# Optimization experiments

Measured on AMD Instinct MI355X. Metric: run time of the kernel, lower is better.

## Reference

```python
import jax, jax.numpy as jnp
import numpy as np

B, N, F, FE, H, C = 2, 2048, 128, 8, 4, 64
LEAKY_ALPHA = 0.2
NEG_INF = -1e9


def setup_inputs() -> dict:
    key = jax.random.key(0)
    ks = jax.random.split(key, 8)
    return {
        "X": jax.random.normal(ks[0], (B, N, F), jnp.float32),
        "A": jax.random.uniform(ks[1], (B, N, N), jnp.float32),
        "E": jax.random.normal(ks[2], (B, N, N, FE), jnp.float32),
        "W_edge": jax.random.normal(ks[3], (FE, 1), jnp.float32) * 0.1,
        "b_edge": jnp.zeros((1,), jnp.float32),
        "W_gat": jax.random.normal(ks[4], (H, F, C), jnp.float32) * 0.05,
        "a_src": jax.random.normal(ks[5], (H, C), jnp.float32) * 0.1,
        "a_dst": jax.random.normal(ks[6], (H, C), jnp.float32) * 0.1,
        "b_gat": jnp.zeros((H * C,), jnp.float32),
        "ln_gamma": jnp.ones((H * C,), jnp.float32),
        "ln_beta": jnp.zeros((H * C,), jnp.float32),
    }


def reference(X, A, E, W_edge, b_edge, W_gat, a_src, a_dst, b_gat, ln_gamma, ln_beta):
    # --- edge gate: sigmoid(Dense_1(E)) -> [B,N,N], multiply into adjacency ---
    edge_w = jax.nn.sigmoid(jnp.einsum("bije,eo->bijo", E, W_edge) + b_edge)
    A = A * edge_w[..., 0]  # [B,N,N]

    # --- multi-head dense GAT (spektral GATConv, concat_heads, elu) ---
    h = jnp.einsum("bnf,hfc->bnhc", X, W_gat)  # [B,N,H,C]
    s_src = jnp.einsum("bnhc,hc->bnh", h, a_src)  # [B,N,H]
    s_dst = jnp.einsum("bnhc,hc->bnh", h, a_dst)
    # e_ij = LeakyReLU(src_i + dst_j): [B,N(i),N(j),H]
    logits = jax.nn.leaky_relu(s_src[:, :, None, :] + s_dst[:, None, :, :],
                               negative_slope=LEAKY_ALPHA)
    mask = jnp.where(A == 0.0, NEG_INF, 0.0)[..., None]  # [B,N,N,1]
    attn = jax.nn.softmax(logits + mask, axis=2)  # softmax over neighbors j
    out = jnp.einsum("bijh,bjhc->bihc", attn, h)  # [B,N,H,C]
    out = out.reshape(B, N, H * C) + b_gat
    out = jax.nn.elu(out)

    # --- LayerNorm over the feature axis (inference: dropout is identity) ---
    mu = jnp.mean(out, axis=-1, keepdims=True)
    var = jnp.var(out, axis=-1, keepdims=True)
    out = (out - mu) * jax.lax.rsqrt(var + 1e-3) * ln_gamma + ln_beta
    return out
```

## Files before the change

### kernel.cpp

```cpp
#include <hip/hip_runtime.h>
#include <hip/hip_bf16.h>


#define BB 2
#define NN 2048
#define FF 128
#define HH 4
#define CC 64
#define HC 256
#define TN 8
#define JB (NN / 8)
#define LOG2E 1.4426950408889634f

typedef __attribute__((ext_vector_type(8))) short short8;
typedef __attribute__((ext_vector_type(4))) float f32x4;

__device__ __forceinline__ float wave_sum(float v) {
#pragma unroll
    for (int m = 32; m >= 1; m >>= 1) v += __shfl_xor(v, m, 64);
    return v;
}

__device__ __forceinline__ unsigned short bf16rne(float x) {
    unsigned u = __float_as_uint(x);
    return (unsigned short)((u + 0x7fffu + ((u >> 16) & 1u)) >> 16);
}

__global__ __launch_bounds__(256) void k1_proj(
    const float* __restrict__ X, const float* __restrict__ Adj,
    const float* __restrict__ Wg,
    const float* __restrict__ a_src, const float* __restrict__ a_dst,
    unsigned short* __restrict__ hT, float* __restrict__ ssT,
    float* __restrict__ sdT, unsigned char* __restrict__ zT)
{
    const int blk = blockIdx.x;
    const int b  = blk / (NN / TN);
    const int n0 = (blk % (NN / TN)) * TN;
    const int tid = threadIdx.x;
    const int h = tid >> 6, c = tid & 63;

    float hv[TN];
#pragma unroll
    for (int r = 0; r < TN; ++r) hv[r] = 0.f;

    const float* xp = X + (size_t)(b * NN + n0) * FF;

#pragma unroll 4
    for (int f4 = 0; f4 < FF / 4; ++f4) {
        const int f = f4 * 4;
        const float w0 = Wg[(h * FF + f + 0) * CC + c];
        const float w1 = Wg[(h * FF + f + 1) * CC + c];
        const float w2 = Wg[(h * FF + f + 2) * CC + c];
        const float w3 = Wg[(h * FF + f + 3) * CC + c];
#pragma unroll
        for (int r = 0; r < TN; ++r) {
            float4 x4 = *(const float4*)(xp + r * FF + f);
            hv[r] = fmaf(x4.x, w0, hv[r]);
            hv[r] = fmaf(x4.y, w1, hv[r]);
            hv[r] = fmaf(x4.z, w2, hv[r]);
            hv[r] = fmaf(x4.w, w3, hv[r]);
        }
    }

    union { short8 v; unsigned short u[8]; } pk;
#pragma unroll
    for (int r = 0; r < TN; ++r) pk.u[r] = bf16rne(hv[r]);
    *(short8*)&hT[((((size_t)b * HH + h) * JB + (n0 >> 3)) * CC + c) * 8] = pk.v;

    const float as = a_src[tid];
    const float ad = a_dst[tid];
#pragma unroll
    for (int r = 0; r < TN; ++r) {
        const int n = n0 + r;
        float s1 = wave_sum(hv[r] * as);
        float s2 = wave_sum(hv[r] * ad);
        if (c == 0) {
            ssT[(b * HH + h) * NN + n] = s1 * LOG2E;
            sdT[(b * HH + h) * NN + n] = s2 * LOG2E;
        }
    }

    {
        const int r = tid >> 5;
        const int s = tid & 31;
        const size_t row = (size_t)(b * NN + n0 + r);
        const float* ap = Adj + row * NN + s * 64;
        unsigned char* zp = zT + (row << 8);
#pragma unroll
        for (int k = 0; k < 8; ++k) {
            float4 a0 = *(const float4*)(ap + k * 8);
            float4 a1 = *(const float4*)(ap + k * 8 + 4);
            unsigned m = 0u;
            m |= (a0.x == 0.f) ? 1u   : 0u;
            m |= (a0.y == 0.f) ? 2u   : 0u;
            m |= (a0.z == 0.f) ? 4u   : 0u;
            m |= (a0.w == 0.f) ? 8u   : 0u;
            m |= (a1.x == 0.f) ? 16u  : 0u;
            m |= (a1.y == 0.f) ? 32u  : 0u;
            m |= (a1.z == 0.f) ? 64u  : 0u;
            m |= (a1.w == 0.f) ? 128u : 0u;
            const int jb = s * 8 + k;
            const int jq = jb >> 6, rem = jb & 63;
            const int it = rem >> 2, lq = rem & 3;
            zp[jq * 64 + lq * 16 + it] = (unsigned char)m;
        }
    }
}

struct Stage {
    float4 sda, sdb;
    short8 bfr[4];
};

__device__ __forceinline__ void load_stage(
    Stage& s, const float* sdp, const unsigned short* hb, int it)
{
    const int js = it * 32;
    s.sda = *(const float4*)(sdp + js);
    s.sdb = *(const float4*)(sdp + js + 4);
    const unsigned short* hp = hb + it * 2048;
#pragma unroll
    for (int ni = 0; ni < 4; ++ni)
        s.bfr[ni] = *(const short8*)(hp + ni * 128);
}

__device__ __forceinline__ void consume_stage(
    const Stage& s, float ss, bool wz,
    unsigned long long mlo, unsigned long long mhi, int it,
    f32x4* acc, f32x4& accS, short8 onesv)
{
    const float sd[8] = {s.sda.x, s.sda.y, s.sda.z, s.sda.w,
                         s.sdb.x, s.sdb.y, s.sdb.z, s.sdb.w};
    float p[8];
    __builtin_amdgcn_s_setprio(1);
#pragma unroll
    for (int t = 0; t < 8; ++t) {
        float x = ss + sd[t];
        x = fmaxf(x, 0.2f * x);
        p[t] = __builtin_amdgcn_exp2f(x);
    }
    if (wz) {
        const unsigned mb =
            (unsigned)(((it & 8) ? mhi : mlo) >> ((it & 7) * 8)) & 0xffu;
        if (__any(mb != 0u)) {
#pragma unroll
            for (int t = 0; t < 8; ++t)
                if ((mb >> t) & 1u) p[t] = 0.f;
        }
    }
    union { short8 v; __hip_bfloat162 h2[4]; } pk;
#pragma unroll
    for (int t = 0; t < 4; ++t)
        pk.h2[t] = __float22bfloat162_rn(make_float2(p[2 * t], p[2 * t + 1]));
    accS = __builtin_amdgcn_mfma_f32_16x16x32_bf16(pk.v, onesv, accS, 0, 0, 0);
#pragma unroll
    for (int ni = 0; ni < 4; ++ni)
        acc[ni] = __builtin_amdgcn_mfma_f32_16x16x32_bf16(pk.v, s.bfr[ni], acc[ni], 0, 0, 0);
    __builtin_amdgcn_s_setprio(0);
}

__global__ __launch_bounds__(1024, 4) void k2_attn(
    const unsigned short* __restrict__ hT, const float* __restrict__ ssT,
    const float* __restrict__ sdT, const unsigned char* __restrict__ zT,
    const float* __restrict__ b_gat, const float* __restrict__ gamma,
    const float* __restrict__ beta, float* __restrict__ out)
{
    __shared__ float accs[3][16][HH][64];
    __shared__ float lsumx[4][HH][16];

    const int blk = blockIdx.x;
    const int b  = blk >> 7;
    const int i0 = (blk & 127) << 4;
    const int tid  = threadIdx.x;
    const int wave = tid >> 6;
    const int h  = wave & 3;
    const int jq = wave >> 2;
    const int l  = tid & 63;
    const int lr = l & 15;
    const int lq = l >> 4;

    const float ss = ssT[(b * HH + h) * NN + i0 + lr];

    const uint4 mw = *(const uint4*)(zT + ((size_t)(b * NN + i0 + lr) << 8)
                                       + jq * 64 + lq * 16);
    const unsigned long long mlo = ((unsigned long long)mw.y << 32) | mw.x;
    const unsigned long long mhi = ((unsigned long long)mw.w << 32) | mw.z;
    const bool wz = __any((mlo | mhi) != 0ull);

    short8 onesv;
#pragma unroll
    for (int i = 0; i < 8; ++i) onesv[i] = (short)0x3F80;

    f32x4 acc[4];
#pragma unroll
    for (int ni = 0; ni < 4; ++ni) acc[ni] = (f32x4){0.f, 0.f, 0.f, 0.f};
    f32x4 accS = (f32x4){0.f, 0.f, 0.f, 0.f};

    const float* sdp = sdT + (b * HH + h) * NN + jq * 512 + lq * 8;
    const unsigned short* hb =
        hT + ((((size_t)b * HH + h) * JB + jq * 64 + lq) * CC + lr) * 8;

    Stage s0, s1;
    load_stage(s0, sdp, hb, 0);
    load_stage(s1, sdp, hb, 1);
#pragma unroll 1
    for (int it = 0; it < 16; it += 2) {
        consume_stage(s0, ss, wz, mlo, mhi, it, acc, accS, onesv);
        if (it + 2 < 16) load_stage(s0, sdp, hb, it + 2);
        consume_stage(s1, ss, wz, mlo, mhi, it + 1, acc, accS, onesv);
        if (it + 3 < 16) load_stage(s1, sdp, hb, it + 3);
    }

    if (lr == 0)
#pragma unroll
        for (int r = 0; r < 4; ++r) lsumx[jq][h][lq * 4 + r] = accS[r];

    if (jq > 0) {
#pragma unroll
        for (int ni = 0; ni < 4; ++ni)
#pragma unroll
            for (int r = 0; r < 4; ++r)
                accs[jq - 1][ni * 4 + r][h][l] = acc[ni][r];
    }
    __syncthreads();

    float vals[4][4];
    if (jq == 0) {
        const float lcomb = lsumx[0][h][lr] + lsumx[1][h][lr]
                          + lsumx[2][h][lr] + lsumx[3][h][lr];
        float lrow[4];
#pragma unroll
        for (int r = 0; r < 4; ++r) lrow[r] = __shfl(lcomb, lq * 4 + r, 64);

        float bg[4];
#pragma unroll
        for (int ni = 0; ni < 4; ++ni) bg[ni] = b_gat[h * 64 + ni * 16 + lr];

#pragma unroll
        for (int ni = 0; ni < 4; ++ni)
#pragma unroll
            for (int r = 0; r < 4; ++r) {
                float a = acc[ni][r] + accs[0][ni * 4 + r][h][l]
                        + accs[1][ni * 4 + r][h][l] + accs[2][ni * 4 + r][h][l];
                float v = a / lrow[r] + bg[ni];
                vals[ni][r] = (v > 0.f) ? v : (__expf(v) - 1.f);
            }
    }
    __syncthreads();

    float* vbuf = &accs[0][0][0][0];
    if (jq == 0) {
#pragma unroll
        for (int ni = 0; ni < 4; ++ni)
#pragma unroll
            for (int r = 0; r < 4; ++r)
                vbuf[((h * 4 + ni) * 16 + (lq * 4 + r)) * 16 + lr] = vals[ni][r];
    }
    __syncthreads();

    {
        const int row = wave;
        const int h2  = l >> 4;
        const int ni2 = (l >> 2) & 3;
        const int lr0 = (l & 3) * 4;
        float4 v4 = *(const float4*)&vbuf[((h2 * 4 + ni2) * 16 + row) * 16 + lr0];

        float S1 = wave_sum(v4.x + v4.y + v4.z + v4.w);
        float S2 = wave_sum(v4.x * v4.x + v4.y * v4.y + v4.z * v4.z + v4.w * v4.w);
        float mu  = S1 * (1.f / HC);
        float var = S2 * (1.f / HC) - mu * mu;
        float inv = rsqrtf(var + 1e-3f);

        float4 gm = *(const float4*)&gamma[l * 4];
        float4 bm = *(const float4*)&beta[l * 4];
        float4 o;
        o.x = (v4.x - mu) * inv * gm.x + bm.x;
        o.y = (v4.y - mu) * inv * gm.y + bm.y;
        o.z = (v4.z - mu) * inv * gm.z + bm.z;
        o.w = (v4.w - mu) * inv * gm.w + bm.w;
        *(float4*)(out + (size_t)(b * NN + i0 + row) * HC + l * 4) = o;
    }
}

extern "C" void kernel_launch(void* const* d_in, const int* in_sizes, int n_in,
                              void* d_out, int out_size, void* d_ws, size_t ws_size,
                              hipStream_t stream)
{
    const float* X     = (const float*)d_in[0];
    const float* Adj   = (const float*)d_in[1];
    const float* Wg    = (const float*)d_in[5];
    const float* a_src = (const float*)d_in[6];
    const float* a_dst = (const float*)d_in[7];
    const float* b_gat = (const float*)d_in[8];
    const float* gam   = (const float*)d_in[9];
    const float* bet   = (const float*)d_in[10];
    float* out = (float*)d_out;

    const size_t hT_elems = (size_t)BB * HH * CC * NN;
    const size_t ss_elems = (size_t)BB * HH * NN;

    unsigned short* hT = (unsigned short*)d_ws;
    float* ssT = (float*)(hT + hT_elems);
    float* sdT = ssT + ss_elems;
    unsigned char* zT = (unsigned char*)(sdT + ss_elems);

    k1_proj<<<BB * NN / TN, 256, 0, stream>>>(X, Adj, Wg, a_src, a_dst, hT, ssT, sdT, zT);
    k2_attn<<<BB * (NN / 16), 1024, 0, stream>>>(hT, ssT, sdT, zT, b_gat, gam, bet, out);
}
```

Measured before the change: 370.4 us.

## Split attention blocks by j-quarter across row tiles and reduce partials in new kernel

Each attention block used to cover 16 rows with four waves splitting the neighbor range, then combine the four partial sums in shared memory and apply the norm. Now each block covers 64 rows for a single neighbor quarter, so the four row subgroups share the same hT and sdT stream, which improves reuse of those loads. Partial numerators and denominators are written to global workspace, and a third kernel sums them, then applies bias, ELU and LayerNorm. This drops the in-block syncs and shared-memory reduction, at the cost of an extra launch and roughly 16 MB of partial-sum traffic to global memory.

```diff
diff --git a/kernel.cpp b/kernel.cpp
--- a/kernel.cpp
+++ b/kernel.cpp
@@ -162,27 +162,26 @@
 __global__ __launch_bounds__(1024, 4) void k2_attn(
     const unsigned short* __restrict__ hT, const float* __restrict__ ssT,
     const float* __restrict__ sdT, const unsigned char* __restrict__ zT,
-    const float* __restrict__ b_gat, const float* __restrict__ gamma,
-    const float* __restrict__ beta, float* __restrict__ out)
-{
-    __shared__ float accs[3][16][HH][64];
-    __shared__ float lsumx[4][HH][16];
-
+    float* __restrict__ Pacc, float* __restrict__ Pden)
+{
     const int blk = blockIdx.x;
-    const int b  = blk >> 7;
-    const int i0 = (blk & 127) << 4;
+    const int b     = blk >> 7;
+    const int itile = (blk >> 2) & 31;
+    const int jqB   = blk & 3;
+    const int i0    = itile * 64;
     const int tid  = threadIdx.x;
     const int wave = tid >> 6;
-    const int h  = wave & 3;
-    const int jq = wave >> 2;
+    const int h    = wave & 3;
+    const int isub = wave >> 2;
     const int l  = tid & 63;
     const int lr = l & 15;
     const int lq = l >> 4;
-
-    const float ss = ssT[(b * HH + h) * NN + i0 + lr];
-
-    const uint4 mw = *(const uint4*)(zT + ((size_t)(b * NN + i0 + lr) << 8)
-                                       + jq * 64 + lq * 16);
+    const int irow0 = i0 + isub * 16;
+
+    const float ss = ssT[(b * HH + h) * NN + irow0 + lr];
+
+    const uint4 mw = *(const uint4*)(zT + ((size_t)(b * NN + irow0 + lr) << 8)
+                                       + jqB * 64 + lq * 16);
     const unsigned long long mlo = ((unsigned long long)mw.y << 32) | mw.x;
     const unsigned long long mhi = ((unsigned long long)mw.w << 32) | mw.z;
     const bool wz = __any((mlo | mhi) != 0ull);
@@ -196,9 +195,9 @@
     for (int ni = 0; ni < 4; ++ni) acc[ni] = (f32x4){0.f, 0.f, 0.f, 0.f};
     f32x4 accS = (f32x4){0.f, 0.f, 0.f, 0.f};
 
-    const float* sdp = sdT + (b * HH + h) * NN + jq * 512 + lq * 8;
+    const float* sdp = sdT + (b * HH + h) * NN + jqB * 512 + lq * 8;
     const unsigned short* hb =
-        hT + ((((size_t)b * HH + h) * JB + jq * 64 + lq) * CC + lr) * 8;
+        hT + ((((size_t)b * HH + h) * JB + jqB * 64 + lq) * CC + lr) * 8;
 
     Stage s0, s1;
     load_stage(s0, sdp, hb, 0);
@@ -211,74 +210,86 @@
         if (it + 3 < 16) load_stage(s1, sdp, hb, it + 3);
     }
 
-    if (lr == 0)
-#pragma unroll
-        for (int r = 0; r < 4; ++r) lsumx[jq][h][lq * 4 + r] = accS[r];
-
-    if (jq > 0) {
-#pragma unroll
-        for (int ni = 0; ni < 4; ++ni)
-#pragma unroll
-            for (int r = 0; r < 4; ++r)
-                accs[jq - 1][ni * 4 + r][h][l] = acc[ni][r];
-    }
-    __syncthreads();
-
-    float vals[4][4];
-    if (jq == 0) {
-        const float lcomb = lsumx[0][h][lr] + lsumx[1][h][lr]
-                          + lsumx[2][h][lr] + lsumx[3][h][lr];
-        float lrow[4];
-#pragma unroll
-        for (int r = 0; r < 4; ++r) lrow[r] = __shfl(lcomb, lq * 4 + r, 64);
-
-        float bg[4];
-#pragma unroll
-        for (int ni = 0; ni < 4; ++ni) bg[ni] = b_gat[h * 64 + ni * 16 + lr];
-
-#pragma unroll
-        for (int ni = 0; ni < 4; ++ni)
-#pragma unroll
-            for (int r = 0; r < 4; ++r) {
-                float a = acc[ni][r] + accs[0][ni * 4 + r][h][l]
-                        + accs[1][ni * 4 + r][h][l] + accs[2][ni * 4 + r][h][l];
-                float v = a / lrow[r] + bg[ni];
-                vals[ni][r] = (v > 0.f) ? v : (__expf(v) - 1.f);
-            }
-    }
-    __syncthreads();
-
-    float* vbuf = &accs[0][0][0][0];
-    if (jq == 0) {
-#pragma unroll
-        for (int ni = 0; ni < 4; ++ni)
-#pragma unroll
-            for (int r = 0; r < 4; ++r)
-                vbuf[((h * 4 + ni) * 16 + (lq * 4 + r)) * 16 + lr] = vals[ni][r];
-    }
-    __syncthreads();
-
-    {
-        const int row = wave;
-        const int h2  = l >> 4;
-        const int ni2 = (l >> 2) & 3;
-        const int lr0 = (l & 3) * 4;
-        float4 v4 = *(const float4*)&vbuf[((h2 * 4 + ni2) * 16 + row) * 16 + lr0];
-
-        float S1 = wave_sum(v4.x + v4.y + v4.z + v4.w);
-        float S2 = wave_sum(v4.x * v4.x + v4.y * v4.y + v4.z * v4.z + v4.w * v4.w);
-        float mu  = S1 * (1.f / HC);
-        float var = S2 * (1.f / HC) - mu * mu;
-        float inv = rsqrtf(var + 1e-3f);
-
-        float4 gm = *(const float4*)&gamma[l * 4];
-        float4 bm = *(const float4*)&beta[l * 4];
+    float* pa = Pacc + (((size_t)(b * 4 + jqB) * NN + irow0) * HC) + h * 64 + lr;
+#pragma unroll
+    for (int ni = 0; ni < 4; ++ni)
+#pragma unroll
+        for (int r = 0; r < 4; ++r)
+            pa[(size_t)(lq * 4 + r) * HC + ni * 16] = acc[ni][r];
+    if (lr == 0) {
+        float* pd = Pden + ((size_t)(b * 4 + jqB) * NN + irow0) * HH + h;
+#pragma unroll
+        for (int r = 0; r < 4; ++r) pd[(lq * 4 + r) * HH] = accS[r];
+    }
+}
+
+__global__ __launch_bounds__(256) void k3_norm(
+    const float* __restrict__ Pacc, const float* __restrict__ Pden,
+    const float* __restrict__ b_gat, const float* __restrict__ gamma,
+    const float* __restrict__ beta, float* __restrict__ out)
+{
+    const int blk = blockIdx.x;
+    const int b  = blk >> 7;
+    const int i0 = (blk & 127) << 4;
+    const int tid = threadIdx.x;
+    const int row = tid >> 4;
+    const int q   = tid & 15;
+    const int i   = i0 + row;
+    const int h   = q >> 2;
+
+    float4 s[4];
+#pragma unroll
+    for (int k = 0; k < 4; ++k) s[k] = make_float4(0.f, 0.f, 0.f, 0.f);
+    float d = 0.f;
+
+#pragma unroll
+    for (int jq = 0; jq < 4; ++jq) {
+        const float* pa = Pacc + ((size_t)(b * 4 + jq) * NN + i) * HC + q * 16;
+#pragma unroll
+        for (int k = 0; k < 4; ++k) {
+            float4 v = *(const float4*)(pa + k * 4);
+            s[k].x += v.x; s[k].y += v.y; s[k].z += v.z; s[k].w += v.w;
+        }
+        d += Pden[((size_t)(b * 4 + jq) * NN + i) * HH + h];
+    }
+
+    const float invd = 1.f / d;
+    float vv[16];
+    float S1 = 0.f, S2 = 0.f;
+#pragma unroll
+    for (int k = 0; k < 4; ++k) {
+        float4 bg = *(const float4*)(b_gat + q * 16 + k * 4);
+        float e[4] = {s[k].x, s[k].y, s[k].z, s[k].w};
+        float g[4] = {bg.x, bg.y, bg.z, bg.w};
+#pragma unroll
+        for (int t = 0; t < 4; ++t) {
+            float v = e[t] * invd + g[t];
+            v = (v > 0.f) ? v : (__expf(v) - 1.f);
+            vv[k * 4 + t] = v;
+            S1 += v;
+            S2 += v * v;
+        }
+    }
+#pragma unroll
+    for (int m = 1; m <= 8; m <<= 1) {
+        S1 += __shfl_xor(S1, m, 64);
+        S2 += __shfl_xor(S2, m, 64);
+    }
+    const float mu  = S1 * (1.f / HC);
+    const float var = S2 * (1.f / HC) - mu * mu;
+    const float inv = rsqrtf(var + 1e-3f);
+
+    float* op = out + (size_t)(b * NN + i) * HC + q * 16;
+#pragma unroll
+    for (int k = 0; k < 4; ++k) {
+        float4 gm = *(const float4*)(gamma + q * 16 + k * 4);
+        float4 bm = *(const float4*)(beta  + q * 16 + k * 4);
         float4 o;
-        o.x = (v4.x - mu) * inv * gm.x + bm.x;
-        o.y = (v4.y - mu) * inv * gm.y + bm.y;
-        o.z = (v4.z - mu) * inv * gm.z + bm.z;
-        o.w = (v4.w - mu) * inv * gm.w + bm.w;
-        *(float4*)(out + (size_t)(b * NN + i0 + row) * HC + l * 4) = o;
+        o.x = (vv[k * 4 + 0] - mu) * inv * gm.x + bm.x;
+        o.y = (vv[k * 4 + 1] - mu) * inv * gm.y + bm.y;
+        o.z = (vv[k * 4 + 2] - mu) * inv * gm.z + bm.z;
+        o.w = (vv[k * 4 + 3] - mu) * inv * gm.w + bm.w;
+        *(float4*)(op + k * 4) = o;
     }
 }
 
@@ -298,12 +309,16 @@
 
     const size_t hT_elems = (size_t)BB * HH * CC * NN;
     const size_t ss_elems = (size_t)BB * HH * NN;
+    const size_t zT_bytes = (size_t)BB * NN * 256;
 
     unsigned short* hT = (unsigned short*)d_ws;
     float* ssT = (float*)(hT + hT_elems);
     float* sdT = ssT + ss_elems;
     unsigned char* zT = (unsigned char*)(sdT + ss_elems);
+    float* Pacc = (float*)(zT + zT_bytes);
+    float* Pden = Pacc + (size_t)BB * 4 * NN * HC;
 
     k1_proj<<<BB * NN / TN, 256, 0, stream>>>(X, Adj, Wg, a_src, a_dst, hT, ssT, sdT, zT);
-    k2_attn<<<BB * (NN / 16), 1024, 0, stream>>>(hT, ssT, sdT, zT, b_gat, gam, bet, out);
-}
+    k2_attn<<<BB * (NN / 16), 1024, 0, stream>>>(hT, ssT, sdT, zT, Pacc, Pden);
+    k3_norm<<<BB * (NN / 16), 256, 0, stream>>>(Pacc, Pden, b_gat, gam, bet, out);
+}
```

After: 375.8 us. About the same (+1.5%).

## Split attention neighbor range across two wave groups with four-deep prefetch

Applied to the files above, without the earlier changes.

Shrinks the attention block from 16 to 8 waves, so each wave covers 1024 neighbors over 32 iterations instead of 512 over 16. The loads are now four-stage double buffered instead of two-stage, and mask bytes are extracted once per group of four stages. The cross-wave reduction drops from four partials to two, and the LayerNorm epilogue is remapped so each wave handles two rows with half-wave shuffles. This cuts LDS reduction traffic and gives more prefetch depth, at the cost of less parallelism per block and higher register pressure from four live stages.

```diff
diff --git a/kernel.cpp b/kernel.cpp
--- a/kernel.cpp
+++ b/kernel.cpp
@@ -125,8 +125,7 @@
 }
 
 __device__ __forceinline__ void consume_stage(
-    const Stage& s, float ss, bool wz,
-    unsigned long long mlo, unsigned long long mhi, int it,
+    const Stage& s, float ss, bool wz, unsigned mb,
     f32x4* acc, f32x4& accS, short8 onesv)
 {
     const float sd[8] = {s.sda.x, s.sda.y, s.sda.z, s.sda.w,
@@ -140,8 +139,6 @@
         p[t] = __builtin_amdgcn_exp2f(x);
     }
     if (wz) {
-        const unsigned mb =
-            (unsigned)(((it & 8) ? mhi : mlo) >> ((it & 7) * 8)) & 0xffu;
         if (__any(mb != 0u)) {
 #pragma unroll
             for (int t = 0; t < 8; ++t)
@@ -159,14 +156,14 @@
     __builtin_amdgcn_s_setprio(0);
 }
 
-__global__ __launch_bounds__(1024, 4) void k2_attn(
+__global__ __launch_bounds__(512, 2) void k2_attn(
     const unsigned short* __restrict__ hT, const float* __restrict__ ssT,
     const float* __restrict__ sdT, const unsigned char* __restrict__ zT,
     const float* __restrict__ b_gat, const float* __restrict__ gamma,
     const float* __restrict__ beta, float* __restrict__ out)
 {
-    __shared__ float accs[3][16][HH][64];
-    __shared__ float lsumx[4][HH][16];
+    __shared__ float accs[16][HH][64];
+    __shared__ float lsumx[2][HH][16];
 
     const int blk = blockIdx.x;
     const int b  = blk >> 7;
@@ -174,18 +171,22 @@
     const int tid  = threadIdx.x;
     const int wave = tid >> 6;
     const int h  = wave & 3;
-    const int jq = wave >> 2;
+    const int jh = wave >> 2;
     const int l  = tid & 63;
     const int lr = l & 15;
     const int lq = l >> 4;
 
     const float ss = ssT[(b * HH + h) * NN + i0 + lr];
 
-    const uint4 mw = *(const uint4*)(zT + ((size_t)(b * NN + i0 + lr) << 8)
-                                       + jq * 64 + lq * 16);
-    const unsigned long long mlo = ((unsigned long long)mw.y << 32) | mw.x;
-    const unsigned long long mhi = ((unsigned long long)mw.w << 32) | mw.z;
-    const bool wz = __any((mlo | mhi) != 0ull);
+    const unsigned char* zp = zT + ((size_t)(b * NN + i0 + lr) << 8)
+                                 + jh * 128 + lq * 16;
+    const uint4 mwa = *(const uint4*)(zp);
+    const uint4 mwb = *(const uint4*)(zp + 64);
+    const unsigned long long m0 = ((unsigned long long)mwa.y << 32) | mwa.x;
+    const unsigned long long m1 = ((unsigned long long)mwa.w << 32) | mwa.z;
+    const unsigned long long m2 = ((unsigned long long)mwb.y << 32) | mwb.x;
+    const unsigned long long m3 = ((unsigned long long)mwb.w << 32) | mwb.z;
+    const bool wz = __any((m0 | m1 | m2 | m3) != 0ull);
 
     short8 onesv;
 #pragma unroll
@@ -196,38 +197,50 @@
     for (int ni = 0; ni < 4; ++ni) acc[ni] = (f32x4){0.f, 0.f, 0.f, 0.f};
     f32x4 accS = (f32x4){0.f, 0.f, 0.f, 0.f};
 
-    const float* sdp = sdT + (b * HH + h) * NN + jq * 512 + lq * 8;
+    const float* sdp = sdT + (b * HH + h) * NN + jh * 1024 + lq * 8;
     const unsigned short* hb =
-        hT + ((((size_t)b * HH + h) * JB + jq * 64 + lq) * CC + lr) * 8;
-
-    Stage s0, s1;
+        hT + ((((size_t)b * HH + h) * JB + jh * 128 + lq) * CC + lr) * 8;
+
+    Stage s0, s1, s2, s3;
     load_stage(s0, sdp, hb, 0);
     load_stage(s1, sdp, hb, 1);
+    load_stage(s2, sdp, hb, 2);
+    load_stage(s3, sdp, hb, 3);
 #pragma unroll 1
-    for (int it = 0; it < 16; it += 2) {
-        consume_stage(s0, ss, wz, mlo, mhi, it, acc, accS, onesv);
-        if (it + 2 < 16) load_stage(s0, sdp, hb, it + 2);
-        consume_stage(s1, ss, wz, mlo, mhi, it + 1, acc, accS, onesv);
-        if (it + 3 < 16) load_stage(s1, sdp, hb, it + 3);
+    for (int it = 0; it < 32; it += 4) {
+        const unsigned long long msel = (it & 16) ? ((it & 8) ? m3 : m2)
+                                                  : ((it & 8) ? m1 : m0);
+        const int sh = (it & 7) * 8;
+        const unsigned mb0 = (unsigned)(msel >> sh) & 0xffu;
+        const unsigned mb1 = (unsigned)(msel >> (sh + 8)) & 0xffu;
+        const unsigned mb2 = (unsigned)(msel >> (sh + 16)) & 0xffu;
+        const unsigned mb3 = (unsigned)(msel >> (sh + 24)) & 0xffu;
+        consume_stage(s0, ss, wz, mb0, acc, accS, onesv);
+        if (it + 4 < 32) load_stage(s0, sdp, hb, it + 4);
+        consume_stage(s1, ss, wz, mb1, acc, accS, onesv);
+        if (it + 5 < 32) load_stage(s1, sdp, hb, it + 5);
+        consume_stage(s2, ss, wz, mb2, acc, accS, onesv);
+        if (it + 6 < 32) load_stage(s2, sdp, hb, it + 6);
+        consume_stage(s3, ss, wz, mb3, acc, accS, onesv);
+        if (it + 7 < 32) load_stage(s3, sdp, hb, it + 7);
     }
 
     if (lr == 0)
 #pragma unroll
-        for (int r = 0; r < 4; ++r) lsumx[jq][h][lq * 4 + r] = accS[r];
-
-    if (jq > 0) {
+        for (int r = 0; r < 4; ++r) lsumx[jh][h][lq * 4 + r] = accS[r];
+
+    if (jh == 1) {
 #pragma unroll
         for (int ni = 0; ni < 4; ++ni)
 #pragma unroll
             for (int r = 0; r < 4; ++r)
-                accs[jq - 1][ni * 4 + r][h][l] = acc[ni][r];
+                accs[ni * 4 + r][h][l] = acc[ni][r];
     }
     __syncthreads();
 
     float vals[4][4];
-    if (jq == 0) {
-        const float lcomb = lsumx[0][h][lr] + lsumx[1][h][lr]
-                          + lsumx[2][h][lr] + lsumx[3][h][lr];
+    if (jh == 0) {
+        const float lcomb = lsumx[0][h][lr] + lsumx[1][h][lr];
         float lrow[4];
 #pragma unroll
         for (int r = 0; r < 4; ++r) lrow[r] = __shfl(lcomb, lq * 4 + r, 64);
@@ -240,16 +253,15 @@
         for (int ni = 0; ni < 4; ++ni)
 #pragma unroll
             for (int r = 0; r < 4; ++r) {
-                float a = acc[ni][r] + accs[0][ni * 4 + r][h][l]
-                        + accs[1][ni * 4 + r][h][l] + accs[2][ni * 4 + r][h][l];
+                float a = acc[ni][r] + accs[ni * 4 + r][h][l];
                 float v = a / lrow[r] + bg[ni];
                 vals[ni][r] = (v > 0.f) ? v : (__expf(v) - 1.f);
             }
     }
     __syncthreads();
 
-    float* vbuf = &accs[0][0][0][0];
-    if (jq == 0) {
+    float* vbuf = &accs[0][0][0];
+    if (jh == 0) {
 #pragma unroll
         for (int ni = 0; ni < 4; ++ni)
 #pragma unroll
@@ -259,26 +271,43 @@
     __syncthreads();
 
     {
-        const int row = wave;
-        const int h2  = l >> 4;
-        const int ni2 = (l >> 2) & 3;
-        const int lr0 = (l & 3) * 4;
-        float4 v4 = *(const float4*)&vbuf[((h2 * 4 + ni2) * 16 + row) * 16 + lr0];
-
-        float S1 = wave_sum(v4.x + v4.y + v4.z + v4.w);
-        float S2 = wave_sum(v4.x * v4.x + v4.y * v4.y + v4.z * v4.z + v4.w * v4.w);
-        float mu  = S1 * (1.f / HC);
-        float var = S2 * (1.f / HC) - mu * mu;
-        float inv = rsqrtf(var + 1e-3f);
-
-        float4 gm = *(const float4*)&gamma[l * 4];
-        float4 bm = *(const float4*)&beta[l * 4];
-        float4 o;
-        o.x = (v4.x - mu) * inv * gm.x + bm.x;
-        o.y = (v4.y - mu) * inv * gm.y + bm.y;
-        o.z = (v4.z - mu) * inv * gm.z + bm.z;
-        o.w = (v4.w - mu) * inv * gm.w + bm.w;
-        *(float4*)(out + (size_t)(b * NN + i0 + row) * HC + l * 4) = o;
+        const int row = wave * 2 + (l >> 5);
+        const int hl  = l & 31;
+        const int c0  = hl >> 1;
+        const int o0  = (hl & 1) * 8;
+        const float* vp = &vbuf[(c0 * 16 + row) * 16 + o0];
+        float4 va = *(const float4*)vp;
+        float4 vb = *(const float4*)(vp + 4);
+
+        float S1 = va.x + va.y + va.z + va.w + vb.x + vb.y + vb.z + vb.w;
+        float S2 = va.x * va.x + va.y * va.y + va.z * va.z + va.w * va.w
+                 + vb.x * vb.x + vb.y * vb.y + vb.z * vb.z + vb.w * vb.w;
+#pragma unroll
+        for (int m = 1; m <= 16; m <<= 1) {
+            S1 += __shfl_xor(S1, m, 64);
+            S2 += __shfl_xor(S2, m, 64);
+        }
+        const float mu  = S1 * (1.f / HC);
+        const float var = S2 * (1.f / HC) - mu * mu;
+        const float inv = rsqrtf(var + 1e-3f);
+
+        const int f0 = hl * 8;
+        float4 g0 = *(const float4*)(gamma + f0);
+        float4 g1 = *(const float4*)(gamma + f0 + 4);
+        float4 b0 = *(const float4*)(beta + f0);
+        float4 b1 = *(const float4*)(beta + f0 + 4);
+        float4 oa, ob;
+        oa.x = (va.x - mu) * inv * g0.x + b0.x;
+        oa.y = (va.y - mu) * inv * g0.y + b0.y;
+        oa.z = (va.z - mu) * inv * g0.z + b0.z;
+        oa.w = (va.w - mu) * inv * g0.w + b0.w;
+        ob.x = (vb.x - mu) * inv * g1.x + b1.x;
+        ob.y = (vb.y - mu) * inv * g1.y + b1.y;
+        ob.z = (vb.z - mu) * inv * g1.z + b1.z;
+        ob.w = (vb.w - mu) * inv * g1.w + b1.w;
+        float* op = out + (size_t)(b * NN + i0 + row) * HC + f0;
+        *(float4*)op = oa;
+        *(float4*)(op + 4) = ob;
     }
 }
 
@@ -305,5 +334,5 @@
     unsigned char* zT = (unsigned char*)(sdT + ss_elems);
 
     k1_proj<<<BB * NN / TN, 256, 0, stream>>>(X, Adj, Wg, a_src, a_dst, hT, ssT, sdT, zT);
-    k2_attn<<<BB * (NN / 16), 1024, 0, stream>>>(hT, ssT, sdT, zT, b_gat, gam, bet, out);
-}
+    k2_attn<<<BB * (NN / 16), 512, 0, stream>>>(hT, ssT, sdT, zT, b_gat, gam, bet, out);
+}
```

Result: no change. 370.3 us (-0.0%).
